# Optimization experiments

Hardware: AMD Instinct MI355X
Metric: run time of the kernel (lower is better)

Reference implementation:

```python
import jax, jax.numpy as jnp
import numpy as np

B, L, D, H = 4, 2048, 1024, 16
HD = D // H  # head_dim = 64


def setup_inputs() -> dict:
    key = jax.random.key(0)
    k1, k2, k3 = jax.random.split(key, 3)
    x = jax.random.normal(k1, (B, L, D), dtype=jnp.float32)
    # causal mask: True where attention is NOT allowed (masked_fill semantics)
    mask = ~jnp.tril(jnp.ones((L, L), dtype=bool))
    Wqkv = jax.random.normal(k2, (3 * D, D), dtype=jnp.float32) * (1.0 / np.sqrt(D))
    bqkv = jnp.zeros((3 * D,), dtype=jnp.float32)
    Wo = jax.random.normal(k3, (D, D), dtype=jnp.float32) * (1.0 / np.sqrt(D))
    bo = jnp.zeros((D,), dtype=jnp.float32)
    return {"x": x, "mask": mask, "Wqkv": Wqkv, "bqkv": bqkv, "Wo": Wo, "bo": bo}


def reference(x, mask, Wqkv, bqkv, Wo, bo):
    b, l, d = x.shape
    qkv = jnp.einsum('bld,ed->ble', x, Wqkv) + bqkv            # [b, l, 3d]
    q, k, v = jnp.split(qkv, 3, axis=-1)
    q = q.reshape(b, l, H, HD).transpose(0, 2, 1, 3)           # [b, h, l, hd]
    k = k.reshape(b, l, H, HD).transpose(0, 2, 1, 3)
    v = v.reshape(b, l, H, HD).transpose(0, 2, 1, 3)
    scale = 1.0 / jnp.sqrt(jnp.float32(HD))
    a = jnp.einsum('bhqd,bhkd->bhqk', q, k) * scale            # [b, h, l, l]
    a = jnp.where(mask, -jnp.inf, a)
    a = jax.nn.softmax(a, axis=-1)
    out = jnp.einsum('bhqk,bhkd->bhqd', a, v)                  # [b, h, l, hd]
    out = out.transpose(0, 2, 1, 3).reshape(b, l, d)
    return jnp.einsum('bld,ed->ble', out, Wo) + bo
```

## Files before the change

### kernel.cpp

```cpp
#include <hip/hip_runtime.h>

typedef __attribute__((ext_vector_type(8))) short short8;
typedef __attribute__((ext_vector_type(4))) float f32x4;
typedef __attribute__((ext_vector_type(16))) float f32x16;
typedef __attribute__((ext_vector_type(2))) int int2v;
typedef __attribute__((ext_vector_type(4))) int int4v;
typedef unsigned short u16;
typedef unsigned int u32;

#define B_ 4
#define L_ 2048
#define D_ 1024
#define H_ 16
#define HD_ 64


__device__ __forceinline__ u16 f2bf(float f) {
  union { float f; unsigned u; } c; c.f = f;
  unsigned r = c.u + 0x7FFFu + ((c.u >> 16) & 1u);
  return (u16)(r >> 16);
}

__device__ __forceinline__ u32 cvtpk(float a, float b) {
  u32 r; asm("v_cvt_pk_bf16_f32 %0, %1, %2" : "=v"(r) : "v"(a), "v"(b)); return r;
}

#define TRREAD(dst, base, OFFLIT) \
  asm volatile("ds_read_b64_tr_b16 %0, %1 offset:" OFFLIT \
               : "=v"(dst) : "v"(base) : "memory")

__device__ __forceinline__ void pswap(u32& a, u32& b) {
  asm("v_permlane32_swap_b32 %0, %1" : "+v"(a), "+v"(b));
}

__global__ __launch_bounds__(256) void cvt_all(const float* __restrict__ x,
                                               const float* __restrict__ wqkv,
                                               const float* __restrict__ wo,
                                               u16* __restrict__ out) {
  const long n1 = (long)B_ * L_ * D_;
  const long n2 = (long)3 * D_ * D_;
  long i = ((long)blockIdx.x * 256 + threadIdx.x) * 4;
  const float* src;
  long off;
  if (i < n1) { src = x; off = i; }
  else if (i < n1 + n2) { src = wqkv; off = i - n1; }
  else { src = wo; off = i - n1 - n2; }
  float4 v = *(const float4*)(src + off);
  u16 o0 = f2bf(v.x), o1 = f2bf(v.y), o2 = f2bf(v.z), o3 = f2bf(v.w);
  u16* p = out + i;
  p[0] = o0; p[1] = o1; p[2] = o2; p[3] = o3;
}

template <int QCOLS, bool BF16_OUT>
__global__ __launch_bounds__(256, 3) void gemm_bt(
    const u16* __restrict__ A, const u16* __restrict__ B,
    const float* __restrict__ bias, void* __restrict__ Cout,
    int M, int N, int K) {
  __shared__ u16 Asm[128 * 64];
  __shared__ u16 Bsm[128 * 64];
  const int tid = threadIdx.x;
  const int lane = tid & 63;
  const int wid = tid >> 6;
  const int fr = lane & 15, fq = lane >> 4;
  const int wr = wid >> 1, wc = wid & 1;

  const int nwg = gridDim.x;
  const int cpx = nwg >> 3;
  const int id = (blockIdx.x & 7) * cpx + (blockIdx.x >> 3);
  const int NBX = N >> 7;
  const long n0 = (long)(id % NBX) * 128;
  const long m0 = (long)(id / NBX) * 128;

  const int srl = lane >> 3;
  const int sgc = ((lane & 7) ^ srl) * 8;

  const u16* gA[4];
  const u16* gB[4];
  u32 ldst[4];
#pragma unroll
  for (int c = 0; c < 4; ++c) {
    const int row = c * 32 + wid * 8 + srl;
    gA[c] = A + (m0 + row) * K + sgc;
    gB[c] = B + (n0 + row) * K + sgc;
    ldst[c] = (u32)((c * 256 + wid * 64) * 16 + lane * 16);
  }

  f32x4 acc[4][4] = {};
  short8 rA[4], rB[4];
#pragma unroll
  for (int c = 0; c < 4; ++c) {
    rA[c] = *(const short8*)(gA[c]);
    rB[c] = *(const short8*)(gB[c]);
  }

  for (int kt = 0; kt < K; kt += 64) {
    __syncthreads();
#pragma unroll
    for (int c = 0; c < 4; ++c) {
      *(short8*)((char*)Asm + ldst[c]) = rA[c];
      *(short8*)((char*)Bsm + ldst[c]) = rB[c];
    }
    __syncthreads();
    if (kt + 64 < K) {
#pragma unroll
      for (int c = 0; c < 4; ++c) {
        rA[c] = *(const short8*)(gA[c] + kt + 64);
        rB[c] = *(const short8*)(gB[c] + kt + 64);
      }
    }
#pragma unroll
    for (int ks = 0; ks < 2; ++ks) {
      short8 af[4], bfr[4];
#pragma unroll
      for (int m = 0; m < 4; ++m) {
        const int row = wr * 64 + m * 16 + fr;
        af[m] = *(const short8*)((const char*)Asm + row * 128 +
                                 (((ks * 4 + fq) ^ (row & 7)) * 16));
      }
#pragma unroll
      for (int n = 0; n < 4; ++n) {
        const int row = wc * 64 + n * 16 + fr;
        bfr[n] = *(const short8*)((const char*)Bsm + row * 128 +
                                  (((ks * 4 + fq) ^ (row & 7)) * 16));
      }
#pragma unroll
      for (int m = 0; m < 4; ++m)
#pragma unroll
        for (int n = 0; n < 4; ++n)
          acc[m][n] = __builtin_amdgcn_mfma_f32_16x16x32_bf16(af[m], bfr[n], acc[m][n], 0, 0, 0);
    }
  }

  float bv[4];
#pragma unroll
  for (int n = 0; n < 4; ++n) bv[n] = bias[n0 + wc * 64 + n * 16 + fr];

#pragma unroll
  for (int m = 0; m < 4; ++m) {
#pragma unroll
    for (int n = 0; n < 4; ++n) {
      const long col = n0 + wc * 64 + n * 16 + fr;
      const float sc = (QCOLS > 0 && col < QCOLS) ? 0.18033688f : 1.0f;
#pragma unroll
      for (int r = 0; r < 4; ++r) {
        const long row = m0 + wr * 64 + m * 16 + fq * 4 + r;
        float v = (acc[m][n][r] + bv[n]) * sc;
        if (BF16_OUT)
          ((u16*)Cout)[row * N + col] = f2bf(v);
        else
          ((float*)Cout)[row * N + col] = v;
      }
    }
  }
}

__global__ __launch_bounds__(256, 4) void flash_attn18(
    const u16* __restrict__ qkv, u16* __restrict__ attn) {
  __shared__ u16 K1[64 * 64];
  __shared__ u16 V1[64 * 64];

  const int tid = threadIdx.x;
  const int lane = tid & 63;
  const int wid = tid >> 6;
  const int l31 = lane & 31;
  const int h = lane >> 5;

  const int bh = blockIdx.x;
  const int y = blockIdx.y;
  const int qt = (y < 4) ? 15 - y : (y < 8) ? y + 4 : (y < 12) ? 15 - y : y - 12;
  const long rowbase = (long)(bh >> 4) * L_;
  const int hh = bh & 15;

  const int wq0 = qt * 128 + wid * 32;
  const int qg = wq0 + l31;

  short8 qf[4];
  {
    const u16* qp = qkv + (rowbase + qg) * 3072 + hh * 64 + h * 8;
#pragma unroll
    for (int ks = 0; ks < 4; ++ks) qf[ks] = *(const short8*)(qp + ks * 16);
  }

  short8 ones;
#pragma unroll
  for (int j = 0; j < 8; ++j) ones[j] = (short)0x3F80;

  const u16* gK[2];
  const u16* gV[2];
  u32 dstKV[2];
#pragma unroll
  for (int c = 0; c < 2; ++c) {
    const int s = (wid * 2 + c) * 8 + (lane >> 3);
    const int kvv = ((s >> 2) << 2) + ((lane >> 1) & 3);
    const int dvv = ((s & 3) << 4) + ((lane & 1) << 3);
    const int kchunk = ((lane & 7) ^ (lane >> 3)) * 8;
    gK[c] = qkv + (rowbase + s) * 3072 + 1024 + hh * 64 + kchunk;
    gV[c] = qkv + (rowbase + kvv) * 3072 + 2048 + hh * 64 + dvv;
    dstKV[c] = (u32)((wid * 2 + c) * 1024 + lane * 16);
  }

  const u32 Vaddr = (u32)(unsigned long long)(__attribute__((address_space(3))) char*)(void*)&V1[0];
  const u32 vb0 = Vaddr + ((lane >> 4) & 1) * 128 + (lane & 15) * 8 + h * 1024;

  f32x16 o[2] = {};
  float l_r = 0.f;

  short8 stK[2], stV[2];
#pragma unroll
  for (int c = 0; c < 2; ++c) {
    stK[c] = *(const short8*)(gK[c]);
    stV[c] = *(const short8*)(gV[c]);
  }

  const int ktm = 2 * qt + 1;
  for (int kt = 0; kt <= ktm; ++kt) {
    __syncthreads();
#pragma unroll
    for (int c = 0; c < 2; ++c) {
      *(short8*)((char*)K1 + dstKV[c]) = stK[c];
      *(short8*)((char*)V1 + dstKV[c]) = stV[c];
    }
    __syncthreads();
    if (kt < ktm) {
      const long goff = (long)(kt + 1) * 64 * 3072;
#pragma unroll
      for (int c = 0; c < 2; ++c) {
        stK[c] = *(const short8*)(gK[c] + goff);
        stV[c] = *(const short8*)(gV[c] + goff);
      }
    }
    const int ktb = kt * 64;
    if (ktb <= wq0 + 31) {
      const char* Kb = (const char*)K1;

      f32x16 p[2];
      __builtin_amdgcn_s_setprio(1);
#pragma unroll
      for (int t = 0; t < 2; ++t) {
        f32x16 acc = {};
#pragma unroll
        for (int ks = 0; ks < 4; ++ks) {
          const int row = t * 32 + l31;
          short8 kf = *(const short8*)(Kb + row * 128 + (((ks * 2 + h) ^ (row & 7)) * 16));
          acc = __builtin_amdgcn_mfma_f32_32x32x16_bf16(kf, qf[ks], acc, 0, 0, 0);
        }
        p[t] = acc;
      }
      __builtin_amdgcn_s_setprio(0);

      __builtin_amdgcn_sched_barrier(0);
      int2v vf[16];
      TRREAD(vf[0], vb0, "0");     TRREAD(vf[1], vb0, "512");
      TRREAD(vf[2], vb0, "2048");  TRREAD(vf[3], vb0, "2560");
      TRREAD(vf[4], vb0, "4096");  TRREAD(vf[5], vb0, "4608");
      TRREAD(vf[6], vb0, "6144");  TRREAD(vf[7], vb0, "6656");
      TRREAD(vf[8], vb0, "256");   TRREAD(vf[9], vb0, "768");
      TRREAD(vf[10], vb0, "2304"); TRREAD(vf[11], vb0, "2816");
      TRREAD(vf[12], vb0, "4352"); TRREAD(vf[13], vb0, "4864");
      TRREAD(vf[14], vb0, "6400"); TRREAD(vf[15], vb0, "6912");

      if (ktb + 63 > wq0) {
#pragma unroll
        for (int t = 0; t < 2; ++t)
#pragma unroll
          for (int r = 0; r < 16; ++r) {
            const int kvg = ktb + t * 32 + (r & 3) + 8 * (r >> 2) + 4 * h;
            p[t][r] = (kvg > qg) ? -__builtin_inff() : p[t][r];
          }
      }

#pragma unroll
      for (int t = 0; t < 2; ++t)
#pragma unroll
        for (int r = 0; r < 16; ++r)
          p[t][r] = __builtin_exp2f(p[t][r]);

      u32 pf[4][4];
#pragma unroll
      for (int t = 0; t < 2; ++t)
#pragma unroll
        for (int ksl = 0; ksl < 2; ++ksl) {
          u32 x0 = cvtpk(p[t][8 * ksl + 0], p[t][8 * ksl + 1]);
          u32 x1 = cvtpk(p[t][8 * ksl + 2], p[t][8 * ksl + 3]);
          u32 y0 = cvtpk(p[t][8 * ksl + 4], p[t][8 * ksl + 5]);
          u32 y1 = cvtpk(p[t][8 * ksl + 6], p[t][8 * ksl + 7]);
          pswap(x0, y0);
          pswap(x1, y1);
          const int ks = t * 2 + ksl;
          pf[ks][0] = x0; pf[ks][1] = x1; pf[ks][2] = y0; pf[ks][3] = y1;
        }

      asm volatile("s_waitcnt lgkmcnt(0)" ::: "memory");
      __builtin_amdgcn_sched_barrier(0);
      __builtin_amdgcn_s_setprio(1);
      f32x16 lac = {};
#pragma unroll
      for (int ks = 0; ks < 4; ++ks) {
        int4v pv;
        pv[0] = (int)pf[ks][0]; pv[1] = (int)pf[ks][1];
        pv[2] = (int)pf[ks][2]; pv[3] = (int)pf[ks][3];
        const short8 pvf = __builtin_bit_cast(short8, pv);
        int4v a0;
        a0[0] = vf[ks * 2][0]; a0[1] = vf[ks * 2][1];
        a0[2] = vf[ks * 2 + 1][0]; a0[3] = vf[ks * 2 + 1][1];
        o[0] = __builtin_amdgcn_mfma_f32_32x32x16_bf16(
            __builtin_bit_cast(short8, a0), pvf, o[0], 0, 0, 0);
        int4v a1;
        a1[0] = vf[8 + ks * 2][0]; a1[1] = vf[8 + ks * 2][1];
        a1[2] = vf[8 + ks * 2 + 1][0]; a1[3] = vf[8 + ks * 2 + 1][1];
        o[1] = __builtin_amdgcn_mfma_f32_32x32x16_bf16(
            __builtin_bit_cast(short8, a1), pvf, o[1], 0, 0, 0);
        lac = __builtin_amdgcn_mfma_f32_32x32x16_bf16(ones, pvf, lac, 0, 0, 0);
      }
      __builtin_amdgcn_s_setprio(0);
      l_r += lac[0];
    }
  }

  const float invl = 1.0f / l_r;
  u16* orow = attn + (rowbase + qg) * 1024 + hh * 64;
#pragma unroll
  for (int t = 0; t < 2; ++t)
#pragma unroll
    for (int rp = 0; rp < 8; ++rp) {
      const int r0 = rp * 2;
      const u32 w = cvtpk(o[t][r0] * invl, o[t][r0 + 1] * invl);
      const int d = t * 32 + (r0 & 3) + 8 * (r0 >> 2) + 4 * h;
      *(u32*)(orow + d) = w;
    }
}

extern "C" void kernel_launch(void* const* d_in, const int* in_sizes, int n_in,
                              void* d_out, int out_size, void* d_ws, size_t ws_size,
                              hipStream_t stream) {
  const float* x    = (const float*)d_in[0];
  const float* Wqkv = (const float*)d_in[2];
  const float* bqkv = (const float*)d_in[3];
  const float* Wo   = (const float*)d_in[4];
  const float* bo   = (const float*)d_in[5];
  float* out = (float*)d_out;

  const long ML = (long)B_ * L_;
  u16* xb    = (u16*)d_ws;
  u16* wqkvb = xb + ML * D_;
  u16* wob   = wqkvb + (long)3 * D_ * D_;
  u16* qkv   = wob + (long)D_ * D_;
  u16* attn  = qkv + ML * 3 * D_;

  const long ncvt = ML * D_ + (long)3 * D_ * D_ + (long)D_ * D_;
  cvt_all<<<dim3((int)(ncvt / 1024)), 256, 0, stream>>>(x, Wqkv, Wo, xb);

  gemm_bt<1024, true><<<dim3((3 * D_ / 128) * (int)(ML / 128)), 256, 0, stream>>>(
      xb, wqkvb, bqkv, qkv, (int)ML, 3 * D_, D_);

  flash_attn18<<<dim3(64, 16), 256, 0, stream>>>(qkv, attn);

  gemm_bt<0, false><<<dim3((D_ / 128) * (int)(ML / 128)), 256, 0, stream>>>(
      attn, wob, bo, out, (int)ML, D_, D_);
}
```

Before: 191.4 us.

## Double-buffer K/V shared tiles in flash attention and widen output stores

Shared-memory K and V tiles become double-buffered. The next tile is written into the alternate buffer after compute, so each iteration needs one barrier instead of two. The epilogue packs four bf16 values per 64-bit store instead of two per 32-bit store. This doubles LDS use per block to 32 KB, which may limit occupancy at the requested 4 blocks per CU.

```diff
diff --git a/kernel.cpp b/kernel.cpp
--- a/kernel.cpp
+++ b/kernel.cpp
@@ -5,6 +5,7 @@
 typedef __attribute__((ext_vector_type(16))) float f32x16;
 typedef __attribute__((ext_vector_type(2))) int int2v;
 typedef __attribute__((ext_vector_type(4))) int int4v;
+typedef __attribute__((ext_vector_type(2))) unsigned int u32x2;
 typedef unsigned short u16;
 typedef unsigned int u32;
 
@@ -154,10 +155,10 @@
   }
 }
 
-__global__ __launch_bounds__(256, 4) void flash_attn18(
+__global__ __launch_bounds__(256, 4) void flash_attn19(
     const u16* __restrict__ qkv, u16* __restrict__ attn) {
-  __shared__ u16 K1[64 * 64];
-  __shared__ u16 V1[64 * 64];
+  __shared__ u16 K2[2][64 * 64];
+  __shared__ u16 V2[2][64 * 64];
 
   const int tid = threadIdx.x;
   const int lane = tid & 63;
@@ -199,7 +200,7 @@
     dstKV[c] = (u32)((wid * 2 + c) * 1024 + lane * 16);
   }
 
-  const u32 Vaddr = (u32)(unsigned long long)(__attribute__((address_space(3))) char*)(void*)&V1[0];
+  const u32 Vaddr = (u32)(unsigned long long)(__attribute__((address_space(3))) char*)(void*)&V2[0][0];
   const u32 vb0 = Vaddr + ((lane >> 4) & 1) * 128 + (lane & 15) * 8 + h * 1024;
 
   f32x16 o[2] = {};
@@ -211,16 +212,16 @@
     stK[c] = *(const short8*)(gK[c]);
     stV[c] = *(const short8*)(gV[c]);
   }
+#pragma unroll
+  for (int c = 0; c < 2; ++c) {
+    *(short8*)((char*)&K2[0][0] + dstKV[c]) = stK[c];
+    *(short8*)((char*)&V2[0][0] + dstKV[c]) = stV[c];
+  }
+  __syncthreads();
 
   const int ktm = 2 * qt + 1;
+  int cur = 0;
   for (int kt = 0; kt <= ktm; ++kt) {
-    __syncthreads();
-#pragma unroll
-    for (int c = 0; c < 2; ++c) {
-      *(short8*)((char*)K1 + dstKV[c]) = stK[c];
-      *(short8*)((char*)V1 + dstKV[c]) = stV[c];
-    }
-    __syncthreads();
     if (kt < ktm) {
       const long goff = (long)(kt + 1) * 64 * 3072;
 #pragma unroll
@@ -231,7 +232,8 @@
     }
     const int ktb = kt * 64;
     if (ktb <= wq0 + 31) {
-      const char* Kb = (const char*)K1;
+      const char* Kb = (const char*)&K2[cur][0];
+      const u32 vbB = vb0 + (u32)cur * 8192;
 
       f32x16 p[2];
       __builtin_amdgcn_s_setprio(1);
@@ -250,14 +252,14 @@
 
       __builtin_amdgcn_sched_barrier(0);
       int2v vf[16];
-      TRREAD(vf[0], vb0, "0");     TRREAD(vf[1], vb0, "512");
-      TRREAD(vf[2], vb0, "2048");  TRREAD(vf[3], vb0, "2560");
-      TRREAD(vf[4], vb0, "4096");  TRREAD(vf[5], vb0, "4608");
-      TRREAD(vf[6], vb0, "6144");  TRREAD(vf[7], vb0, "6656");
-      TRREAD(vf[8], vb0, "256");   TRREAD(vf[9], vb0, "768");
-      TRREAD(vf[10], vb0, "2304"); TRREAD(vf[11], vb0, "2816");
-      TRREAD(vf[12], vb0, "4352"); TRREAD(vf[13], vb0, "4864");
-      TRREAD(vf[14], vb0, "6400"); TRREAD(vf[15], vb0, "6912");
+      TRREAD(vf[0], vbB, "0");     TRREAD(vf[1], vbB, "512");
+      TRREAD(vf[2], vbB, "2048");  TRREAD(vf[3], vbB, "2560");
+      TRREAD(vf[4], vbB, "4096");  TRREAD(vf[5], vbB, "4608");
+      TRREAD(vf[6], vbB, "6144");  TRREAD(vf[7], vbB, "6656");
+      TRREAD(vf[8], vbB, "256");   TRREAD(vf[9], vbB, "768");
+      TRREAD(vf[10], vbB, "2304"); TRREAD(vf[11], vbB, "2816");
+      TRREAD(vf[12], vbB, "4352"); TRREAD(vf[13], vbB, "4864");
+      TRREAD(vf[14], vbB, "6400"); TRREAD(vf[15], vbB, "6912");
 
       if (ktb + 63 > wq0) {
 #pragma unroll
@@ -315,6 +317,15 @@
       __builtin_amdgcn_s_setprio(0);
       l_r += lac[0];
     }
+    if (kt < ktm) {
+#pragma unroll
+      for (int c = 0; c < 2; ++c) {
+        *(short8*)((char*)&K2[cur ^ 1][0] + dstKV[c]) = stK[c];
+        *(short8*)((char*)&V2[cur ^ 1][0] + dstKV[c]) = stV[c];
+      }
+    }
+    __syncthreads();
+    cur ^= 1;
   }
 
   const float invl = 1.0f / l_r;
@@ -322,11 +333,13 @@
 #pragma unroll
   for (int t = 0; t < 2; ++t)
 #pragma unroll
-    for (int rp = 0; rp < 8; ++rp) {
-      const int r0 = rp * 2;
-      const u32 w = cvtpk(o[t][r0] * invl, o[t][r0 + 1] * invl);
-      const int d = t * 32 + (r0 & 3) + 8 * (r0 >> 2) + 4 * h;
-      *(u32*)(orow + d) = w;
+    for (int rp = 0; rp < 4; ++rp) {
+      const int r0 = rp * 4;
+      u32x2 ww;
+      ww[0] = cvtpk(o[t][r0] * invl, o[t][r0 + 1] * invl);
+      ww[1] = cvtpk(o[t][r0 + 2] * invl, o[t][r0 + 3] * invl);
+      const int d = t * 32 + 8 * rp + 4 * h;
+      *(u32x2*)(orow + d) = ww;
     }
 }
 
@@ -353,7 +366,7 @@
   gemm_bt<1024, true><<<dim3((3 * D_ / 128) * (int)(ML / 128)), 256, 0, stream>>>(
       xb, wqkvb, bqkv, qkv, (int)ML, 3 * D_, D_);
 
-  flash_attn18<<<dim3(64, 16), 256, 0, stream>>>(qkv, attn);
+  flash_attn19<<<dim3(64, 16), 256, 0, stream>>>(qkv, attn);
 
   gemm_bt<0, false><<<dim3((D_ / 128) * (int)(ML / 128)), 256, 0, stream>>>(
       attn, wob, bo, out, (int)ML, D_, D_);
```

New measurement: 213.4 us. 1.11x slower.
